# Performance work log

Hardware: AMD Instinct MI355X
Metric: run time of the kernel (lower is better)

The kernel has to match this reference:

```python
import jax, jax.numpy as jnp
import numpy as np

# GlobalAttention block from GATESynergy: to_dense_batch -> multi-head
# masked self-attention per graph -> scatter back to sparse + residual.
B, NMAX, DIN, DOUT, H = 512, 160, 128, 128, 4
DH = DOUT // H  # 32
COUNTS = np.where(np.arange(B) % 2 == 0, 96, 160)  # nodes per graph, sum=65536
T = int(COUNTS.sum())


def _xavier(key, dout, din):
    lim = np.sqrt(6.0 / (din + dout)).astype(np.float32)
    return jax.random.uniform(key, (dout, din), jnp.float32, -lim, lim)


def setup_inputs() -> dict:
    key = jax.random.key(0)
    ks = jax.random.split(key, 5)
    batch = jnp.asarray(np.repeat(np.arange(B), COUNTS), dtype=jnp.int32)
    x = jax.random.normal(ks[0], (T, DIN), jnp.float32)
    return {
        "x": x,
        "batch": batch,
        "Wq": _xavier(ks[1], DOUT, DIN), "bq": jnp.zeros((DOUT,), jnp.float32),
        "Wk": _xavier(ks[2], DOUT, DIN), "bk": jnp.zeros((DOUT,), jnp.float32),
        "Wv": _xavier(ks[3], DOUT, DIN), "bv": jnp.zeros((DOUT,), jnp.float32),
        "Wo": _xavier(ks[4], DOUT, DOUT), "bo": jnp.zeros((DOUT,), jnp.float32),
    }


def reference(x, batch, Wq, bq, Wk, bk, Wv, bv, Wo, bo):
    n = x.shape[0]
    # --- to_dense_batch: sparse [T, D] -> dense [B, NMAX, D] + mask ---
    counts = jax.ops.segment_sum(jnp.ones(n, jnp.int32), batch, num_segments=B)
    starts = jnp.cumsum(counts) - counts            # first node index per graph
    pos = jnp.arange(n, dtype=jnp.int32) - starts[batch]  # slot within graph
    x_dense = jnp.zeros((B, NMAX, DIN), x.dtype).at[batch, pos].set(x)
    mask = jnp.zeros((B, NMAX), bool).at[batch, pos].set(True)

    def proj(W, b):  # [B,N,DIN] -> [B,H,N,DH]
        return (x_dense @ W.T + b).reshape(B, NMAX, H, DH).transpose(0, 2, 1, 3)

    q, k, v = proj(Wq, bq), proj(Wk, bk), proj(Wv, bv)
    scores = jnp.einsum('bhnd,bhmd->bhnm', q, k) / jnp.sqrt(jnp.asarray(DH, x.dtype))
    scores = jnp.where(mask[:, None, None, :], scores, -jnp.inf)  # mask keys
    attn = jax.nn.softmax(scores, axis=-1)  # dropout p=0.0 -> identity
    out = jnp.einsum('bhnm,bhmd->bnhd', attn, v).reshape(B, NMAX, DOUT)
    out = out @ Wo.T + bo
    out_sparse = out[batch, pos]  # gather valid nodes back to sparse layout
    return out_sparse + x  # residual: in_channels == out_channels
```

## Files before the change

kernel.cpp:

```cpp
#include <hip/hip_runtime.h>

typedef unsigned short u16;
typedef unsigned int u32;
typedef __attribute__((ext_vector_type(8))) short bf16x8;
typedef __attribute__((ext_vector_type(4))) float f32x4;

__device__ __forceinline__ u16 f2bf(float f) {
  u32 u = __builtin_bit_cast(u32, f);
  u += 0x7fffu + ((u >> 16) & 1u);
  return (u16)(u >> 16);
}
__device__ __forceinline__ short f2bs(float f) { return (short)f2bf(f); }

__device__ __forceinline__ bf16x8 cvt8(const float* p) {
  f32x4 a = *reinterpret_cast<const f32x4*>(p);
  f32x4 b = *reinterpret_cast<const f32x4*>(p + 4);
  bf16x8 r;
  r[0] = f2bs(a[0]); r[1] = f2bs(a[1]); r[2] = f2bs(a[2]); r[3] = f2bs(a[3]);
  r[4] = f2bs(b[0]); r[5] = f2bs(b[1]); r[6] = f2bs(b[2]); r[7] = f2bs(b[3]);
  return r;
}
__device__ __forceinline__ bf16x8 lds8(const u16* p) {
  return *reinterpret_cast<const bf16x8*>(p);
}

#define MFMA(a, b, c) __builtin_amdgcn_mfma_f32_16x16x32_bf16((a), (b), (c), 0, 0, 0)

constexpr int DIN = 128, DOUT = 128, DH = 32;
constexpr int T = 65536;
constexpr size_t WFOFF = 0;
constexpr size_t QOFF = 65536;
constexpr size_t KOFF = QOFF + (size_t)4 * T * DH;
constexpr size_t VOFF = KOFF + (size_t)4 * T * DH;
constexpr size_t OOFF = VOFF + (size_t)4 * T * DH;
constexpr size_t WS_NEED = (OOFF + (size_t)T * DOUT) * 2;

__device__ __forceinline__ size_t fragoff(int mat, int ft, int ks) {
  return ((size_t)((mat * 8 + ft) * 4 + ks)) << 9;
}

__global__ void cvtw_kernel(const float* __restrict__ Wq, const float* __restrict__ Wk,
                            const float* __restrict__ Wv, const float* __restrict__ Wo,
                            u16* __restrict__ wf) {
  const int fl = blockIdx.x * 256 + threadIdx.x;
  const int lane = fl & 63, ks = (fl >> 6) & 3, ft = (fl >> 8) & 7, mat = fl >> 11;
  const float* src = mat == 0 ? Wq : mat == 1 ? Wk : mat == 2 ? Wv : Wo;
  const int lr = lane & 15, lg = lane >> 4;
  bf16x8 r = cvt8(src + (ft * 16 + lr) * DIN + ks * 32 + lg * 8);
  *reinterpret_cast<bf16x8*>(wf + (size_t)fl * 8) = r;
}

__global__ __launch_bounds__(256, 2) void qkv_kernel(const float* __restrict__ x,
                                                     const float* __restrict__ bq,
                                                     const float* __restrict__ bk,
                                                     const float* __restrict__ bv,
                                                     u16* __restrict__ ws) {
  const int tid = threadIdx.x;
  const int w = tid >> 6, lane = tid & 63, lg = lane >> 4, lr = lane & 15;
  const size_t rbase = (size_t)blockIdx.x * 256 + w * 64;
  const f32x4 zero = {0.f, 0.f, 0.f, 0.f};
  const u16* wf = ws + WFOFF;
  u16* Q = ws + QOFF;
  u16* K = ws + KOFF;
  u16* V = ws + VOFF;

  bf16x8 xa[4][4];
#pragma unroll
  for (int rt = 0; rt < 4; ++rt)
#pragma unroll
    for (int ks = 0; ks < 4; ++ks)
      xa[rt][ks] = cvt8(x + (rbase + rt * 16 + lr) * DIN + ks * 32 + lg * 8);

#pragma unroll
  for (int ft = 0; ft < 8; ++ft) {
    const int h = ft >> 1, dt = ft & 1;
    bf16x8 wqf[4], wkf[4], wvf[4];
#pragma unroll
    for (int ks = 0; ks < 4; ++ks) {
      wqf[ks] = lds8(wf + fragoff(0, ft, ks) + lane * 8);
      wkf[ks] = lds8(wf + fragoff(1, ft, ks) + lane * 8);
      wvf[ks] = lds8(wf + fragoff(2, ft, ks) + lane * 8);
    }
    f32x4 qacc[4], kacc[4], vacc[4];
#pragma unroll
    for (int rt = 0; rt < 4; ++rt) qacc[rt] = kacc[rt] = vacc[rt] = zero;
#pragma unroll
    for (int rt = 0; rt < 4; ++rt)
#pragma unroll
      for (int ks = 0; ks < 4; ++ks) {
        qacc[rt] = MFMA(xa[rt][ks], wqf[ks], qacc[rt]);
        kacc[rt] = MFMA(xa[rt][ks], wkf[ks], kacc[rt]);
        vacc[rt] = MFMA(wvf[ks], xa[rt][ks], vacc[rt]);
      }
    const float bqv = bq[ft * 16 + lr], bkv = bk[ft * 16 + lr];
    float bvj[4];
#pragma unroll
    for (int j = 0; j < 4; ++j) bvj[j] = bv[ft * 16 + lg * 4 + j];
#pragma unroll
    for (int rt = 0; rt < 4; ++rt) {
      const size_t row0 = rbase + rt * 16;
      const size_t qk_base = (size_t)h * T * DH + (row0 + lg * 4) * DH + dt * 16 + lr;
      const size_t v_base = (size_t)h * T * DH + (((rbase >> 5) + (rt >> 1)) << 10) +
                            (size_t)(dt * 16 + lg * 4) * 32 + (rt & 1) * 16 + lr;
#pragma unroll
      for (int j = 0; j < 4; ++j) {
        Q[qk_base + (size_t)j * DH] = f2bf(qacc[rt][j] + bqv);
        K[qk_base + (size_t)j * DH] = f2bf(kacc[rt][j] + bkv);
        V[v_base + (size_t)j * 32] = f2bf(vacc[rt][j] + bvj[j]);
      }
    }
  }
}

template <int C>
__device__ void attn_wave(const u16* __restrict__ Qh, const u16* __restrict__ Kh,
                          const u16* __restrict__ Vh, u16* __restrict__ O, int start, int h,
                          int rt, u16 (&strip)[16][168]) {
  constexpr int NT = C / 16, KB = C / 32;
  const int lane = threadIdx.x & 63, lg = lane >> 4, lr = lane & 15;
  const f32x4 zero = {0.f, 0.f, 0.f, 0.f};
  const int gr = start + rt * 16;

  bf16x8 vb[KB][2];
#pragma unroll
  for (int ks = 0; ks < KB; ++ks)
#pragma unroll
    for (int dt = 0; dt < 2; ++dt)
      vb[ks][dt] = lds8(Vh + (((size_t)(start >> 5) + ks) << 10) +
                        (size_t)(dt * 16 + lr) * 32 + lg * 8);

  const bf16x8 qa = lds8(Qh + (size_t)(gr + lr) * DH + lg * 8);
  f32x4 sacc[NT];
#pragma unroll
  for (int ct = 0; ct < NT; ++ct)
    sacc[ct] = MFMA(qa, lds8(Kh + (size_t)(start + ct * 16 + lr) * DH + lg * 8), zero);

  const float scale = 0.17677669529663687f;
  float m[4], s[4];
#pragma unroll
  for (int j = 0; j < 4; ++j) {
    m[j] = sacc[0][j];
#pragma unroll
    for (int ct = 1; ct < NT; ++ct) m[j] = fmaxf(m[j], sacc[ct][j]);
  }
#pragma unroll
  for (int d = 1; d < 16; d <<= 1) {
#pragma unroll
    for (int j = 0; j < 4; ++j) m[j] = fmaxf(m[j], __shfl_xor(m[j], d, 64));
  }
#pragma unroll
  for (int j = 0; j < 4; ++j) {
    s[j] = 0.f;
#pragma unroll
    for (int ct = 0; ct < NT; ++ct) {
      const float p = __expf((sacc[ct][j] - m[j]) * scale);
      sacc[ct][j] = p;
      s[j] += p;
    }
  }
#pragma unroll
  for (int d = 1; d < 16; d <<= 1) {
#pragma unroll
    for (int j = 0; j < 4; ++j) s[j] += __shfl_xor(s[j], d, 64);
  }
#pragma unroll
  for (int j = 0; j < 4; ++j) {
    const float inv = 1.0f / s[j];
#pragma unroll
    for (int ct = 0; ct < NT; ++ct)
      strip[lg * 4 + j][ct * 16 + lr] = f2bf(sacc[ct][j] * inv);
  }
  asm volatile("s_waitcnt lgkmcnt(0)" ::: "memory");

  f32x4 o0 = zero, o1 = zero;
#pragma unroll
  for (int ks = 0; ks < KB; ++ks) {
    const bf16x8 pa = lds8(&strip[lr][ks * 32 + lg * 8]);
    o0 = MFMA(pa, vb[ks][0], o0);
    o1 = MFMA(pa, vb[ks][1], o1);
  }
#pragma unroll
  for (int j = 0; j < 4; ++j) {
    strip[lg * 4 + j][lr] = f2bf(o0[j]);
    strip[lg * 4 + j][16 + lr] = f2bf(o1[j]);
  }
  asm volatile("s_waitcnt lgkmcnt(0)" ::: "memory");
  const int orow = lane >> 2, oc = (lane & 3) * 8;
  *reinterpret_cast<bf16x8*>(O + (size_t)(gr + orow) * DOUT + h * DH + oc) =
      *reinterpret_cast<const bf16x8*>(&strip[orow][oc]);
}

__global__ __launch_bounds__(256, 3) void attn_kernel(u16* __restrict__ ws) {
  __shared__ u16 strip[4][16][168];
  const int w = threadIdx.x >> 6;
  const int phys = blockIdx.x;
  const int xcd = phys & 7, idx = phys >> 3;
  const int sub = idx & 15;
  const int p = (idx >> 4) * 8 + xcd;
  const int rem = sub * 4 + w;
  const int h = rem >> 4, t = rem & 15;
  const u16* Qh = ws + QOFF + (size_t)h * T * DH;
  const u16* Kh = ws + KOFF + (size_t)h * T * DH;
  const u16* Vh = ws + VOFF + (size_t)h * T * DH;
  u16* O = ws + OOFF;
  if (t < 6)
    attn_wave<96>(Qh, Kh, Vh, O, p * 256, h, t, strip[w]);
  else
    attn_wave<160>(Qh, Kh, Vh, O, p * 256 + 96, h, t - 6, strip[w]);
}

__global__ __launch_bounds__(256, 3) void oproj_kernel(const u16* __restrict__ ws,
                                                       const float* __restrict__ bo,
                                                       const float* __restrict__ x,
                                                       float* __restrict__ out) {
  const u16* Ob = ws + OOFF;
  const u16* wf = ws + WFOFF;
  const int tid = threadIdx.x;
  const int w = tid >> 6, lane = tid & 63, lg = lane >> 4, lr = lane & 15;
  const f32x4 zero = {0.f, 0.f, 0.f, 0.f};
  const size_t rbase = (size_t)blockIdx.x * 128 + w * 32;

  bf16x8 oa[2][4];
#pragma unroll
  for (int r = 0; r < 2; ++r)
#pragma unroll
    for (int ks = 0; ks < 4; ++ks)
      oa[r][ks] = lds8(Ob + (rbase + r * 16 + lr) * DOUT + ks * 32 + lg * 8);

  f32x4 acc[2][8];
#pragma unroll
  for (int r = 0; r < 2; ++r)
#pragma unroll
    for (int jt = 0; jt < 8; ++jt) acc[r][jt] = zero;

#pragma unroll
  for (int jt = 0; jt < 8; ++jt) {
#pragma unroll
    for (int ks = 0; ks < 4; ++ks) {
      const bf16x8 wb = lds8(wf + fragoff(3, jt, ks) + lane * 8);
      acc[0][jt] = MFMA(oa[0][ks], wb, acc[0][jt]);
      acc[1][jt] = MFMA(oa[1][ks], wb, acc[1][jt]);
    }
  }

#pragma unroll
  for (int r = 0; r < 2; ++r) {
#pragma unroll
    for (int jt = 0; jt < 8; ++jt) {
      const int c = jt * 16 + lr;
      const float bias = bo[c];
#pragma unroll
      for (int j = 0; j < 4; ++j) {
        const size_t n = rbase + r * 16 + lg * 4 + j;
        out[n * DOUT + c] = acc[r][jt][j] + bias + x[n * DIN + c];
      }
    }
  }
}

struct SLds1 {
  u16 k[160][40];
  u16 vt[32][168];
  u16 strip[4][16][168];
};

template <int C>
__device__ void attn1(const float* __restrict__ xg, const float* __restrict__ Wq,
                      const float* __restrict__ bq, const float* __restrict__ Wk,
                      const float* __restrict__ bk, const float* __restrict__ Wv,
                      const float* __restrict__ bv, float* __restrict__ og, int h, SLds1& sm) {
  constexpr int NT = C / 16, KB = C / 32, SLOTS = (NT + 3) / 4;
  const int tid = threadIdx.x;
  const int w = tid >> 6, lane = tid & 63, lg = lane >> 4, lr = lane & 15;
  const f32x4 zero = {0.f, 0.f, 0.f, 0.f};

  for (int t = w; t < 2 * NT; t += 4) {
    const int rt = t >> 1, dt = t & 1;
    f32x4 kacc = zero, vacc = zero;
#pragma unroll
    for (int ks = 0; ks < 4; ++ks) {
      bf16x8 xa = cvt8(xg + (rt * 16 + lr) * DIN + ks * 32 + lg * 8);
      bf16x8 wk = cvt8(Wk + (h * DH + dt * 16 + lr) * DIN + ks * 32 + lg * 8);
      bf16x8 wv = cvt8(Wv + (h * DH + dt * 16 + lr) * DIN + ks * 32 + lg * 8);
      kacc = MFMA(xa, wk, kacc);
      vacc = MFMA(wv, xa, vacc);
    }
    const float kb_ = bk[h * DH + dt * 16 + lr];
#pragma unroll
    for (int j = 0; j < 4; ++j) {
      sm.k[rt * 16 + lg * 4 + j][dt * 16 + lr] = f2bf(kacc[j] + kb_);
      sm.vt[dt * 16 + lg * 4 + j][rt * 16 + lr] = f2bf(vacc[j] + bv[h * DH + dt * 16 + lg * 4 + j]);
    }
  }
  __syncthreads();

#pragma unroll
  for (int sl = 0; sl < SLOTS; ++sl) {
    const int rt = w + sl * 4;
    if (rt < NT) {
#pragma unroll
      for (int dt = 0; dt < 2; ++dt) {
        f32x4 qacc = zero;
#pragma unroll
        for (int ks = 0; ks < 4; ++ks) {
          bf16x8 xa = cvt8(xg + (rt * 16 + lr) * DIN + ks * 32 + lg * 8);
          bf16x8 wq = cvt8(Wq + (h * DH + dt * 16 + lr) * DIN + ks * 32 + lg * 8);
          qacc = MFMA(xa, wq, qacc);
        }
        const float bias = bq[h * DH + dt * 16 + lr];
#pragma unroll
        for (int j = 0; j < 4; ++j)
          sm.strip[w][lg * 4 + j][dt * 16 + lr] = f2bf(qacc[j] + bias);
      }
      asm volatile("s_waitcnt lgkmcnt(0)" ::: "memory");
      const bf16x8 qa = lds8(&sm.strip[w][lr][lg * 8]);
      f32x4 sacc[NT];
#pragma unroll
      for (int ct = 0; ct < NT; ++ct)
        sacc[ct] = MFMA(qa, lds8(&sm.k[ct * 16 + lr][lg * 8]), zero);
      const float scale = 0.17677669529663687f;
      float m[4], s[4];
#pragma unroll
      for (int j = 0; j < 4; ++j) {
        m[j] = sacc[0][j];
#pragma unroll
        for (int ct = 1; ct < NT; ++ct) m[j] = fmaxf(m[j], sacc[ct][j]);
      }
#pragma unroll
      for (int d = 1; d < 16; d <<= 1)
#pragma unroll
        for (int j = 0; j < 4; ++j) m[j] = fmaxf(m[j], __shfl_xor(m[j], d, 64));
#pragma unroll
      for (int j = 0; j < 4; ++j) {
        s[j] = 0.f;
#pragma unroll
        for (int ct = 0; ct < NT; ++ct) {
          const float p = __expf((sacc[ct][j] - m[j]) * scale);
          sacc[ct][j] = p;
          s[j] += p;
        }
      }
#pragma unroll
      for (int d = 1; d < 16; d <<= 1)
#pragma unroll
        for (int j = 0; j < 4; ++j) s[j] += __shfl_xor(s[j], d, 64);
#pragma unroll
      for (int j = 0; j < 4; ++j) {
        const float inv = 1.0f / s[j];
#pragma unroll
        for (int ct = 0; ct < NT; ++ct)
          sm.strip[w][lg * 4 + j][ct * 16 + lr] = f2bf(sacc[ct][j] * inv);
      }
      asm volatile("s_waitcnt lgkmcnt(0)" ::: "memory");
      f32x4 o0 = zero, o1 = zero;
#pragma unroll
      for (int ks = 0; ks < KB; ++ks) {
        const bf16x8 pa = lds8(&sm.strip[w][lr][ks * 32 + lg * 8]);
        o0 = MFMA(pa, lds8(&sm.vt[lr][ks * 32 + lg * 8]), o0);
        o1 = MFMA(pa, lds8(&sm.vt[16 + lr][ks * 32 + lg * 8]), o1);
      }
#pragma unroll
      for (int j = 0; j < 4; ++j) {
        const int n = rt * 16 + lg * 4 + j;
        og[n * DOUT + h * DH + lr] = o0[j];
        og[n * DOUT + h * DH + 16 + lr] = o1[j];
      }
    }
  }
}

__global__ __launch_bounds__(256, 3) void fb_k1(const float* __restrict__ x,
                                                const float* __restrict__ Wq,
                                                const float* __restrict__ bq,
                                                const float* __restrict__ Wk,
                                                const float* __restrict__ bk,
                                                const float* __restrict__ Wv,
                                                const float* __restrict__ bv,
                                                float* __restrict__ O) {
  __shared__ SLds1 sm;
  const int bid = blockIdx.x;
  const int g = bid >> 2, h = bid & 3;
  const int p = g >> 1;
  if (g & 1)
    attn1<160>(x + (size_t)(p * 256 + 96) * DIN, Wq, bq, Wk, bk, Wv, bv,
               O + (size_t)(p * 256 + 96) * DOUT, h, sm);
  else
    attn1<96>(x + (size_t)(p * 256) * DIN, Wq, bq, Wk, bk, Wv, bv, O + (size_t)(p * 256) * DOUT,
              h, sm);
}

__global__ __launch_bounds__(256, 4) void fb_k2(float* __restrict__ io, const float* __restrict__ x,
                                                const float* __restrict__ Wo,
                                                const float* __restrict__ bo) {
  const int tid = threadIdx.x;
  const int w = tid >> 6, lane = tid & 63, lg = lane >> 4, lr = lane & 15;
  const f32x4 zero = {0.f, 0.f, 0.f, 0.f};
  const int rbase = blockIdx.x * 128 + w * 32;
  bf16x8 oa[2][4];
#pragma unroll
  for (int r = 0; r < 2; ++r)
#pragma unroll
    for (int ks = 0; ks < 4; ++ks)
      oa[r][ks] = cvt8(io + (size_t)(rbase + r * 16 + lr) * DOUT + ks * 32 + lg * 8);
  f32x4 acc[2][8];
#pragma unroll
  for (int r = 0; r < 2; ++r)
#pragma unroll
    for (int jt = 0; jt < 8; ++jt) acc[r][jt] = zero;
#pragma unroll
  for (int jt = 0; jt < 8; ++jt)
#pragma unroll
    for (int ks = 0; ks < 4; ++ks) {
      const bf16x8 wb = cvt8(Wo + (size_t)(jt * 16 + lr) * DOUT + ks * 32 + lg * 8);
      acc[0][jt] = MFMA(oa[0][ks], wb, acc[0][jt]);
      acc[1][jt] = MFMA(oa[1][ks], wb, acc[1][jt]);
    }
#pragma unroll
  for (int r = 0; r < 2; ++r)
#pragma unroll
    for (int jt = 0; jt < 8; ++jt) {
      const int c = jt * 16 + lr;
      const float bias = bo[c];
#pragma unroll
      for (int j = 0; j < 4; ++j) {
        const size_t n = (size_t)rbase + r * 16 + lg * 4 + j;
        io[n * DOUT + c] = acc[r][jt][j] + bias + x[n * DIN + c];
      }
    }
}

extern "C" void kernel_launch(void* const* d_in, const int* in_sizes, int n_in,
                              void* d_out, int out_size, void* d_ws, size_t ws_size,
                              hipStream_t stream) {
  const float* x = (const float*)d_in[0];
  const float* Wq = (const float*)d_in[2];
  const float* bq = (const float*)d_in[3];
  const float* Wk = (const float*)d_in[4];
  const float* bk = (const float*)d_in[5];
  const float* Wv = (const float*)d_in[6];
  const float* bv = (const float*)d_in[7];
  const float* Wo = (const float*)d_in[8];
  const float* bo = (const float*)d_in[9];
  float* out = (float*)d_out;

  if (ws_size >= WS_NEED) {
    u16* ws = (u16*)d_ws;
    cvtw_kernel<<<dim3(32), dim3(256), 0, stream>>>(Wq, Wk, Wv, Wo, ws);
    qkv_kernel<<<dim3(256), dim3(256), 0, stream>>>(x, bq, bk, bv, ws);
    attn_kernel<<<dim3(4096), dim3(256), 0, stream>>>(ws);
    oproj_kernel<<<dim3(512), dim3(256), 0, stream>>>(ws, bo, x, out);
  } else {
    fb_k1<<<dim3(2048), dim3(256), 0, stream>>>(x, Wq, bq, Wk, bk, Wv, bv, out);
    fb_k2<<<dim3(512), dim3(256), 0, stream>>>(out, x, Wo, bo);
  }
}
```

Baseline: 69.38 us.

## Fuse output projection into attention kernel and halve QKV block rows

The attention kernel is remapped so each block's four waves cover the four heads of one 16-row tile. Their bf16 outputs are assembled in a shared tile and multiplied by Wo in-block, followed by bias and residual. This removes the separate oproj kernel and the round trip of the O buffer through global memory. The QKV kernel also processes 128 rows per block across twice as many blocks for more parallelism. In exchange it adds a block-wide barrier and a small tail GEMM per block.

```diff
diff --git a/kernel.cpp b/kernel.cpp
--- a/kernel.cpp
+++ b/kernel.cpp
@@ -32,8 +32,7 @@
 constexpr size_t QOFF = 65536;
 constexpr size_t KOFF = QOFF + (size_t)4 * T * DH;
 constexpr size_t VOFF = KOFF + (size_t)4 * T * DH;
-constexpr size_t OOFF = VOFF + (size_t)4 * T * DH;
-constexpr size_t WS_NEED = (OOFF + (size_t)T * DOUT) * 2;
+constexpr size_t WS_NEED = (VOFF + (size_t)4 * T * DH) * 2;
 
 __device__ __forceinline__ size_t fragoff(int mat, int ft, int ks) {
   return ((size_t)((mat * 8 + ft) * 4 + ks)) << 9;
@@ -57,16 +56,16 @@
                                                      u16* __restrict__ ws) {
   const int tid = threadIdx.x;
   const int w = tid >> 6, lane = tid & 63, lg = lane >> 4, lr = lane & 15;
-  const size_t rbase = (size_t)blockIdx.x * 256 + w * 64;
+  const size_t rbase = (size_t)blockIdx.x * 128 + w * 32;
   const f32x4 zero = {0.f, 0.f, 0.f, 0.f};
   const u16* wf = ws + WFOFF;
   u16* Q = ws + QOFF;
   u16* K = ws + KOFF;
   u16* V = ws + VOFF;
 
-  bf16x8 xa[4][4];
-#pragma unroll
-  for (int rt = 0; rt < 4; ++rt)
+  bf16x8 xa[2][4];
+#pragma unroll
+  for (int rt = 0; rt < 2; ++rt)
 #pragma unroll
     for (int ks = 0; ks < 4; ++ks)
       xa[rt][ks] = cvt8(x + (rbase + rt * 16 + lr) * DIN + ks * 32 + lg * 8);
@@ -81,11 +80,11 @@
       wkf[ks] = lds8(wf + fragoff(1, ft, ks) + lane * 8);
       wvf[ks] = lds8(wf + fragoff(2, ft, ks) + lane * 8);
     }
-    f32x4 qacc[4], kacc[4], vacc[4];
-#pragma unroll
-    for (int rt = 0; rt < 4; ++rt) qacc[rt] = kacc[rt] = vacc[rt] = zero;
-#pragma unroll
-    for (int rt = 0; rt < 4; ++rt)
+    f32x4 qacc[2], kacc[2], vacc[2];
+#pragma unroll
+    for (int rt = 0; rt < 2; ++rt) qacc[rt] = kacc[rt] = vacc[rt] = zero;
+#pragma unroll
+    for (int rt = 0; rt < 2; ++rt)
 #pragma unroll
       for (int ks = 0; ks < 4; ++ks) {
         qacc[rt] = MFMA(xa[rt][ks], wqf[ks], qacc[rt]);
@@ -97,7 +96,7 @@
 #pragma unroll
     for (int j = 0; j < 4; ++j) bvj[j] = bv[ft * 16 + lg * 4 + j];
 #pragma unroll
-    for (int rt = 0; rt < 4; ++rt) {
+    for (int rt = 0; rt < 2; ++rt) {
       const size_t row0 = rbase + rt * 16;
       const size_t qk_base = (size_t)h * T * DH + (row0 + lg * 4) * DH + dt * 16 + lr;
       const size_t v_base = (size_t)h * T * DH + (((rbase >> 5) + (rt >> 1)) << 10) +
@@ -114,8 +113,8 @@
 
 template <int C>
 __device__ void attn_wave(const u16* __restrict__ Qh, const u16* __restrict__ Kh,
-                          const u16* __restrict__ Vh, u16* __restrict__ O, int start, int h,
-                          int rt, u16 (&strip)[16][168]) {
+                          const u16* __restrict__ Vh, int start, int h, int rt,
+                          u16 (&strip)[16][168], u16 (&otile)[16][136]) {
   constexpr int NT = C / 16, KB = C / 32;
   const int lane = threadIdx.x & 63, lg = lane >> 4, lr = lane & 15;
   const f32x4 zero = {0.f, 0.f, 0.f, 0.f};
@@ -181,80 +180,56 @@
   }
 #pragma unroll
   for (int j = 0; j < 4; ++j) {
-    strip[lg * 4 + j][lr] = f2bf(o0[j]);
-    strip[lg * 4 + j][16 + lr] = f2bf(o1[j]);
-  }
-  asm volatile("s_waitcnt lgkmcnt(0)" ::: "memory");
-  const int orow = lane >> 2, oc = (lane & 3) * 8;
-  *reinterpret_cast<bf16x8*>(O + (size_t)(gr + orow) * DOUT + h * DH + oc) =
-      *reinterpret_cast<const bf16x8*>(&strip[orow][oc]);
-}
-
-__global__ __launch_bounds__(256, 3) void attn_kernel(u16* __restrict__ ws) {
+    otile[lg * 4 + j][h * 32 + lr] = f2bf(o0[j]);
+    otile[lg * 4 + j][h * 32 + 16 + lr] = f2bf(o1[j]);
+  }
+}
+
+__global__ __launch_bounds__(256, 3) void attn_kernel(const u16* __restrict__ ws,
+                                                      const float* __restrict__ bo,
+                                                      const float* __restrict__ x,
+                                                      float* __restrict__ out) {
   __shared__ u16 strip[4][16][168];
-  const int w = threadIdx.x >> 6;
+  __shared__ u16 otile[16][136];
+  const int w = threadIdx.x >> 6, lane = threadIdx.x & 63;
+  const int lg = lane >> 4, lr = lane & 15;
   const int phys = blockIdx.x;
   const int xcd = phys & 7, idx = phys >> 3;
-  const int sub = idx & 15;
+  const int t = idx & 15;
   const int p = (idx >> 4) * 8 + xcd;
-  const int rem = sub * 4 + w;
-  const int h = rem >> 4, t = rem & 15;
+  const int h = w;
   const u16* Qh = ws + QOFF + (size_t)h * T * DH;
   const u16* Kh = ws + KOFF + (size_t)h * T * DH;
   const u16* Vh = ws + VOFF + (size_t)h * T * DH;
-  u16* O = ws + OOFF;
-  if (t < 6)
-    attn_wave<96>(Qh, Kh, Vh, O, p * 256, h, t, strip[w]);
-  else
-    attn_wave<160>(Qh, Kh, Vh, O, p * 256 + 96, h, t - 6, strip[w]);
-}
-
-__global__ __launch_bounds__(256, 3) void oproj_kernel(const u16* __restrict__ ws,
-                                                       const float* __restrict__ bo,
-                                                       const float* __restrict__ x,
-                                                       float* __restrict__ out) {
-  const u16* Ob = ws + OOFF;
+
+  int gr;
+  if (t < 6) {
+    attn_wave<96>(Qh, Kh, Vh, p * 256, h, t, strip[w], otile);
+    gr = p * 256 + t * 16;
+  } else {
+    attn_wave<160>(Qh, Kh, Vh, p * 256 + 96, h, t - 6, strip[w], otile);
+    gr = p * 256 + 96 + (t - 6) * 16;
+  }
+  __syncthreads();
+
   const u16* wf = ws + WFOFF;
-  const int tid = threadIdx.x;
-  const int w = tid >> 6, lane = tid & 63, lg = lane >> 4, lr = lane & 15;
   const f32x4 zero = {0.f, 0.f, 0.f, 0.f};
-  const size_t rbase = (size_t)blockIdx.x * 128 + w * 32;
-
-  bf16x8 oa[2][4];
-#pragma unroll
-  for (int r = 0; r < 2; ++r)
-#pragma unroll
-    for (int ks = 0; ks < 4; ++ks)
-      oa[r][ks] = lds8(Ob + (rbase + r * 16 + lr) * DOUT + ks * 32 + lg * 8);
-
-  f32x4 acc[2][8];
-#pragma unroll
-  for (int r = 0; r < 2; ++r)
-#pragma unroll
-    for (int jt = 0; jt < 8; ++jt) acc[r][jt] = zero;
-
-#pragma unroll
-  for (int jt = 0; jt < 8; ++jt) {
-#pragma unroll
-    for (int ks = 0; ks < 4; ++ks) {
-      const bf16x8 wb = lds8(wf + fragoff(3, jt, ks) + lane * 8);
-      acc[0][jt] = MFMA(oa[0][ks], wb, acc[0][jt]);
-      acc[1][jt] = MFMA(oa[1][ks], wb, acc[1][jt]);
-    }
-  }
-
-#pragma unroll
-  for (int r = 0; r < 2; ++r) {
-#pragma unroll
-    for (int jt = 0; jt < 8; ++jt) {
-      const int c = jt * 16 + lr;
-      const float bias = bo[c];
-#pragma unroll
-      for (int j = 0; j < 4; ++j) {
-        const size_t n = rbase + r * 16 + lg * 4 + j;
-        out[n * DOUT + c] = acc[r][jt][j] + bias + x[n * DIN + c];
-      }
-    }
+  bf16x8 oa[4];
+#pragma unroll
+  for (int ks = 0; ks < 4; ++ks) oa[ks] = lds8(&otile[lr][ks * 32 + lg * 8]);
+  f32x4 acc0 = zero, acc1 = zero;
+#pragma unroll
+  for (int ks = 0; ks < 4; ++ks) {
+    acc0 = MFMA(oa[ks], lds8(wf + fragoff(3, w * 2, ks) + lane * 8), acc0);
+    acc1 = MFMA(oa[ks], lds8(wf + fragoff(3, w * 2 + 1, ks) + lane * 8), acc1);
+  }
+  const int c0 = w * 32 + lr, c1 = w * 32 + 16 + lr;
+  const float b0 = bo[c0], b1 = bo[c1];
+#pragma unroll
+  for (int j = 0; j < 4; ++j) {
+    const size_t n = (size_t)gr + lg * 4 + j;
+    out[n * DOUT + c0] = acc0[j] + b0 + x[n * DIN + c0];
+    out[n * DOUT + c1] = acc1[j] + b1 + x[n * DIN + c1];
   }
 }
 
@@ -446,9 +421,8 @@
   if (ws_size >= WS_NEED) {
     u16* ws = (u16*)d_ws;
     cvtw_kernel<<<dim3(32), dim3(256), 0, stream>>>(Wq, Wk, Wv, Wo, ws);
-    qkv_kernel<<<dim3(256), dim3(256), 0, stream>>>(x, bq, bk, bv, ws);
-    attn_kernel<<<dim3(4096), dim3(256), 0, stream>>>(ws);
-    oproj_kernel<<<dim3(512), dim3(256), 0, stream>>>(ws, bo, x, out);
+    qkv_kernel<<<dim3(512), dim3(256), 0, stream>>>(x, bq, bk, bv, ws);
+    attn_kernel<<<dim3(4096), dim3(256), 0, stream>>>(ws, bo, x, out);
   } else {
     fb_k1<<<dim3(2048), dim3(256), 0, stream>>>(x, Wq, bq, Wk, bk, Wv, bv, out);
     fb_k2<<<dim3(512), dim3(256), 0, stream>>>(out, x, Wo, bo);
```

Result: faster. 59.16 us (-14.7%).
